# Optimization experiments

Measured on AMD Instinct MI355X. Metric: run time of the kernel, lower is better.

## Reference

```python
import jax, jax.numpy as jnp
import numpy as np

NUM_HEADS = 10
DICT = 20  # attention_dictionary_size
BATCH = 262144


def setup_inputs() -> dict:
    key = jax.random.key(0)
    ks = jax.random.split(key, 6)
    x = jax.random.normal(ks[0], (BATCH, DICT), dtype=jnp.float32)
    # torch nn.Linear(20, 200, bias=False) weights: shape [out, in] = [200, 20]
    W1 = jax.random.normal(ks[1], (NUM_HEADS * DICT, DICT), dtype=jnp.float32) * 0.1
    W2 = jax.random.normal(ks[2], (NUM_HEADS * DICT, DICT), dtype=jnp.float32) * 0.1
    W3 = jax.random.normal(ks[3], (NUM_HEADS * DICT, DICT), dtype=jnp.float32) * 0.1
    W4 = jax.random.normal(ks[4], (NUM_HEADS * DICT, DICT), dtype=jnp.float32) * 0.1
    gamma = jax.random.normal(ks[5], (1,), dtype=jnp.float32)
    return {"x": x, "W1": W1, "W2": W2, "W3": W3, "W4": W4, "gamma": gamma}


def reference(x, W1, W2, W3, W4, gamma):
    B = x.shape[0]
    m = 1
    inp = x[:, None, :]                                   # [B, 1, 20]
    # Four bias-free projections: y = x @ W.T -> [B, 1, 200]
    q = (inp @ W1.T).reshape(NUM_HEADS, B, m, DICT)       # faithful .view (mixes batch/head)
    k = (inp @ W2.T).reshape(NUM_HEADS, B, DICT, m)
    v = (inp @ W3.T).reshape(NUM_HEADS, B, m, DICT)
    inner = q @ k                                         # [10, B, 1, 1]
    att = jax.nn.softmax(inner, axis=-1)                  # length-1 softmax -> ones (faithful)
    res = jnp.swapaxes(att, -1, -2) @ v                   # [10, B, 1, 20]
    res = res.reshape(B, m, NUM_HEADS * DICT)             # [B, 1, 200]
    out = jax.nn.relu(gamma * res + inp @ W4.T)           # [B, 1, 200]
    return out
```

## Files before the change

### kernel.cpp

```cpp
#include <hip/hip_runtime.h>


#define BATCH          262144
#define DICT           20
#define COLS           200
#define NTHREADS       256
#define ROWS_PER_BLOCK 128
#define NBLOCKS        (BATCH / ROWS_PER_BLOCK)

__global__ __launch_bounds__(NTHREADS)
void attn_collapsed_kernel(const float* __restrict__ x,
                           const float* __restrict__ W3,
                           const float* __restrict__ W4,
                           const float* __restrict__ gamma,
                           float* __restrict__ out)
{
    __shared__ float4 ldsM[COLS * 5];

    const int t = threadIdx.x;
    const float g = gamma[0];

    const float4* w3 = (const float4*)W3;
    const float4* w4 = (const float4*)W4;
    for (int i = t; i < COLS * 5; i += NTHREADS) {
        float4 a = w3[i], b = w4[i], m;
        m.x = fmaf(g, a.x, b.x);
        m.y = fmaf(g, a.y, b.y);
        m.z = fmaf(g, a.z, b.z);
        m.w = fmaf(g, a.w, b.w);
        ldsM[i] = m;
    }
    __syncthreads();

    const int row     = blockIdx.x * ROWS_PER_BLOCK + (t & 127);
    const int colbase = (t >> 7) * 100;

    float4 xv[5];
    {
        const float4* xr = (const float4*)(x + row * DICT);
#pragma unroll
        for (int i = 0; i < 5; ++i) xv[i] = xr[i];
    }

    float4* op = (float4*)(out + row * COLS + colbase);

#pragma unroll 5
    for (int c = 0; c < 25; ++c) {
        const float4* wp = &ldsM[(colbase + 4 * c) * 5];
        float4 acc;
        float* accp = (float*)&acc;
#pragma unroll
        for (int cc = 0; cc < 4; ++cc) {
            float p0 = 0.f, p1 = 0.f;
#pragma unroll
            for (int kk = 0; kk < 5; ++kk) {
                float4 w = wp[cc * 5 + kk];
                p0 = fmaf(w.x, xv[kk].x, p0);
                p1 = fmaf(w.y, xv[kk].y, p1);
                p0 = fmaf(w.z, xv[kk].z, p0);
                p1 = fmaf(w.w, xv[kk].w, p1);
            }
            accp[cc] = fmaxf(p0 + p1, 0.f);
        }
        op[c] = acc;
    }
}

extern "C" void kernel_launch(void* const* d_in, const int* in_sizes, int n_in,
                              void* d_out, int out_size, void* d_ws, size_t ws_size,
                              hipStream_t stream) {
    const float* x     = (const float*)d_in[0];
    const float* W3    = (const float*)d_in[3];
    const float* W4    = (const float*)d_in[4];
    const float* gamma = (const float*)d_in[5];
    float* out = (float*)d_out;

    attn_collapsed_kernel<<<NBLOCKS, NTHREADS, 0, stream>>>(x, W3, W4, gamma, out);
}
```

Measured before the change: 284.4 us.

## Stage outputs in LDS for coalesced stores, read weights via wave-uniform scalar loads

Each wave now computes 50 output columns for 64 rows, reading the W3/W4 weights directly from global memory with a wave-uniform segment index so the loads can become scalar loads. The gamma*W3+W4 fold is done in registers instead of being precomputed into LDS. Results are written into a padded LDS staging buffer and then stored to global memory with fully coalesced float2 writes. This targets the strided per-thread output stores, at the cost of redundant weight FMAs, an extra LDS round trip, and more blocks, each re-reading the weights.

Measured after the change: 411.0 us. 44.5% more time.

```diff
diff --git a/kernel.cpp b/kernel.cpp
--- a/kernel.cpp
+++ b/kernel.cpp
@@ -1,12 +1,13 @@
 #include <hip/hip_runtime.h>
 
 
-#define BATCH          262144
-#define DICT           20
-#define COLS           200
-#define NTHREADS       256
-#define ROWS_PER_BLOCK 128
-#define NBLOCKS        (BATCH / ROWS_PER_BLOCK)
+#define BATCH    262144
+#define DICT     20
+#define COLS     200
+#define NTHREADS 256
+#define RPB      64
+#define NBLOCKS  (BATCH / RPB)
+#define STRIDE2  101
 
 __global__ __launch_bounds__(NTHREADS)
 void attn_collapsed_kernel(const float* __restrict__ x,
@@ -15,54 +16,57 @@
                            const float* __restrict__ gamma,
                            float* __restrict__ out)
 {
-    __shared__ float4 ldsM[COLS * 5];
+    __shared__ float2 stage[RPB * STRIDE2];
 
-    const int t = threadIdx.x;
+    const int t   = threadIdx.x;
+    const int row = t & 63;
+    const int seg = __builtin_amdgcn_readfirstlane(t >> 6);
     const float g = gamma[0];
 
-    const float4* w3 = (const float4*)W3;
-    const float4* w4 = (const float4*)W4;
-    for (int i = t; i < COLS * 5; i += NTHREADS) {
-        float4 a = w3[i], b = w4[i], m;
-        m.x = fmaf(g, a.x, b.x);
-        m.y = fmaf(g, a.y, b.y);
-        m.z = fmaf(g, a.z, b.z);
-        m.w = fmaf(g, a.w, b.w);
-        ldsM[i] = m;
-    }
-    __syncthreads();
-
-    const int row     = blockIdx.x * ROWS_PER_BLOCK + (t & 127);
-    const int colbase = (t >> 7) * 100;
-
+    const int grow = blockIdx.x * RPB + row;
     float4 xv[5];
     {
-        const float4* xr = (const float4*)(x + row * DICT);
+        const float4* xr = (const float4*)(x + grow * DICT);
 #pragma unroll
         for (int i = 0; i < 5; ++i) xv[i] = xr[i];
     }
 
-    float4* op = (float4*)(out + row * COLS + colbase);
+    const float4* w3 = (const float4*)(W3 + seg * 50 * DICT);
+    const float4* w4 = (const float4*)(W4 + seg * 50 * DICT);
+    float2* srow = &stage[row * STRIDE2 + seg * 25];
 
 #pragma unroll 5
     for (int c = 0; c < 25; ++c) {
-        const float4* wp = &ldsM[(colbase + 4 * c) * 5];
-        float4 acc;
-        float* accp = (float*)&acc;
+        float a0 = 0.f, a1 = 0.f;
 #pragma unroll
-        for (int cc = 0; cc < 4; ++cc) {
-            float p0 = 0.f, p1 = 0.f;
+        for (int k = 0; k < 5; ++k) {
+            float4 u3 = w3[(2 * c) * 5 + k];
+            float4 u4 = w4[(2 * c) * 5 + k];
+            a0 = fmaf(fmaf(g, u3.x, u4.x), xv[k].x, a0);
+            a0 = fmaf(fmaf(g, u3.y, u4.y), xv[k].y, a0);
+            a0 = fmaf(fmaf(g, u3.z, u4.z), xv[k].z, a0);
+            a0 = fmaf(fmaf(g, u3.w, u4.w), xv[k].w, a0);
+            float4 v3 = w3[(2 * c + 1) * 5 + k];
+            float4 v4 = w4[(2 * c + 1) * 5 + k];
+            a1 = fmaf(fmaf(g, v3.x, v4.x), xv[k].x, a1);
+            a1 = fmaf(fmaf(g, v3.y, v4.y), xv[k].y, a1);
+            a1 = fmaf(fmaf(g, v3.z, v4.z), xv[k].z, a1);
+            a1 = fmaf(fmaf(g, v3.w, v4.w), xv[k].w, a1);
+        }
+        float2 r;
+        r.x = fmaxf(a0, 0.f);
+        r.y = fmaxf(a1, 0.f);
+        srow[c] = r;
+    }
+    __syncthreads();
+
+    float2* out2 = (float2*)out + (size_t)blockIdx.x * (RPB * COLS / 2);
 #pragma unroll
-            for (int kk = 0; kk < 5; ++kk) {
-                float4 w = wp[cc * 5 + kk];
-                p0 = fmaf(w.x, xv[kk].x, p0);
-                p1 = fmaf(w.y, xv[kk].y, p1);
-                p0 = fmaf(w.z, xv[kk].z, p0);
-                p1 = fmaf(w.w, xv[kk].w, p1);
-            }
-            accp[cc] = fmaxf(p0 + p1, 0.f);
-        }
-        op[c] = acc;
+    for (int i = 0; i < 25; ++i) {
+        const int h   = t + i * NTHREADS;
+        const int r   = h / 100;
+        const int rem = h - r * 100;
+        out2[h] = stage[r * STRIDE2 + rem];
     }
 }
 
```
